# Performance work log

Hardware: AMD Instinct MI355X
Metric: run time of the kernel (lower is better)

The kernel has to match this reference:

```python
import jax, jax.numpy as jnp
import numpy as np

NUM_GRAPHS = 1024
HIDDEN = 256
N_NODES = 500000


def setup_inputs() -> dict:
    key = jax.random.key(0)
    k1, k2, k3, k4 = jax.random.split(key, 4)
    x = jax.random.normal(k1, (N_NODES, HIDDEN), dtype=jnp.float32)
    batch = jnp.sort(jax.random.randint(k2, (N_NODES,), 0, NUM_GRAPHS, dtype=jnp.int64))
    # attention = nn.Linear(hidden_dim, 1): weight [1, hidden], bias [1]
    bound = 1.0 / np.sqrt(HIDDEN)
    att_w = jax.random.uniform(k3, (HIDDEN, 1), dtype=jnp.float32, minval=-bound, maxval=bound)
    att_b = jax.random.uniform(k4, (1,), dtype=jnp.float32, minval=-bound, maxval=bound)
    return {"x": x, "batch": batch, "att_w": att_w, "att_b": att_b}


def reference(x, batch, att_w, att_b):
    seg = batch.astype(jnp.int32)
    # mean pool: segment sum / counts
    sums = jax.ops.segment_sum(x, seg, num_segments=NUM_GRAPHS)  # [G, H]
    counts = jax.ops.segment_sum(jnp.ones((x.shape[0],), x.dtype), seg, num_segments=NUM_GRAPHS)
    mean_pool = sums / jnp.maximum(counts, 1.0)[:, None]
    # max pool
    max_pool = jax.ops.segment_max(x, seg, num_segments=NUM_GRAPHS)
    # attention-weighted add pool: sigmoid(x @ w + b) * x, segment-summed
    weights = jax.nn.sigmoid(x @ att_w + att_b)  # [N, 1]
    att_pool = jax.ops.segment_sum(x * weights, seg, num_segments=NUM_GRAPHS)
    return jnp.concatenate([mean_pool, max_pool, att_pool], axis=-1)
```

## Files before the change

### kernel.cpp

```cpp
#include <hip/hip_runtime.h>
#include <math.h>

constexpr int NUM_GRAPHS = 1024;
constexpr int HIDDEN     = 256;

__global__ void detect_i32_kernel(const int* __restrict__ words, int n,
                                  int* __restrict__ flag) {
    __shared__ int any_nz;
    if (threadIdx.x == 0) any_nz = 0;
    __syncthreads();
    int acc = 0;
    for (int j = 1 + 2 * (int)threadIdx.x; j < n; j += 2 * (int)blockDim.x)
        acc |= words[j];
    if (acc) atomicOr(&any_nz, 1);
    __syncthreads();
    if (threadIdx.x == 0) *flag = any_nz;
}

__global__ void seg_start_kernel(const int* __restrict__ words, int n,
                                 const int* __restrict__ flag,
                                 int* __restrict__ seg) {
    int i = blockIdx.x * blockDim.x + threadIdx.x;
    if (i >= n) return;
    const bool is32 = (*flag != 0);
    int b    = is32 ? words[i] : words[2 * i];
    int prev = (i == 0) ? -1 : (is32 ? words[i - 1] : words[2 * (i - 1)]);
    for (int g = prev + 1; g <= b; ++g) seg[g] = i;
    if (i == n - 1)
        for (int g = b + 1; g <= NUM_GRAPHS; ++g) seg[g] = n;
}

__global__ __launch_bounds__(256) void pool_kernel(
    const float* __restrict__ x, const float* __restrict__ att_w,
    const float* __restrict__ att_b, const int* __restrict__ seg,
    float* __restrict__ out) {
    const int g    = blockIdx.x;
    const int lane = threadIdx.x & 63;
    const int w    = threadIdx.x >> 6;

    const int s0 = seg[g];
    const int e0 = seg[g + 1];

    const float4* __restrict__ x4 = (const float4*)x;
    const float4 wv = ((const float4*)att_w)[lane];
    const float  bias = att_b[0];

    float sx = 0.f, sy = 0.f, sz = 0.f, sw = 0.f;
    float mx = -INFINITY, my = -INFINITY, mz = -INFINITY, mw = -INFINITY;
    float ax = 0.f, ay = 0.f, az = 0.f, aw = 0.f;

    int i = s0 + w;
    if (i < e0) {
        float4 v = x4[(size_t)i * 64 + lane];
        for (;;) {
            const int inext = i + 4;
            float4 vn;
            const bool has_next = (inext < e0);
            if (has_next) vn = x4[(size_t)inext * 64 + lane];

            float p = v.x * wv.x + v.y * wv.y + v.z * wv.z + v.w * wv.w;
#pragma unroll
            for (int off = 32; off >= 1; off >>= 1)
                p += __shfl_xor(p, off, 64);
            const float sig = 1.0f / (1.0f + __expf(-(p + bias)));

            sx += v.x; sy += v.y; sz += v.z; sw += v.w;
            mx = fmaxf(mx, v.x); my = fmaxf(my, v.y);
            mz = fmaxf(mz, v.z); mw = fmaxf(mw, v.w);
            ax += v.x * sig; ay += v.y * sig; az += v.z * sig; aw += v.w * sig;

            if (!has_next) break;
            v = vn;
            i = inext;
        }
    }

    __shared__ float4 lsum[4][64];
    __shared__ float4 lmax[4][64];
    __shared__ float4 latt[4][64];
    lsum[w][lane] = make_float4(sx, sy, sz, sw);
    lmax[w][lane] = make_float4(mx, my, mz, mw);
    latt[w][lane] = make_float4(ax, ay, az, aw);
    __syncthreads();

    if (w == 0) {
        float4 S = lsum[0][lane], M = lmax[0][lane], A = latt[0][lane];
#pragma unroll
        for (int ww = 1; ww < 4; ++ww) {
            float4 s2 = lsum[ww][lane], m2 = lmax[ww][lane], a2 = latt[ww][lane];
            S.x += s2.x; S.y += s2.y; S.z += s2.z; S.w += s2.w;
            M.x = fmaxf(M.x, m2.x); M.y = fmaxf(M.y, m2.y);
            M.z = fmaxf(M.z, m2.z); M.w = fmaxf(M.w, m2.w);
            A.x += a2.x; A.y += a2.y; A.z += a2.z; A.w += a2.w;
        }
        const int cnt = e0 - s0;
        const float inv = 1.0f / (float)(cnt > 0 ? cnt : 1);
        float4* __restrict__ o = (float4*)(out + (size_t)g * 768);
        o[lane]       = make_float4(S.x * inv, S.y * inv, S.z * inv, S.w * inv);
        o[64 + lane]  = M;
        o[128 + lane] = A;
    }
}

extern "C" void kernel_launch(void* const* d_in, const int* in_sizes, int n_in,
                              void* d_out, int out_size, void* d_ws, size_t ws_size,
                              hipStream_t stream) {
    const float* x           = (const float*)d_in[0];
    const int*   batch_words = (const int*)d_in[1];
    const float* att_w       = (const float*)d_in[2];
    const float* att_b       = (const float*)d_in[3];
    float*       out         = (float*)d_out;
    const int n = in_sizes[1];

    int* flag = (int*)d_ws;
    int* seg  = ((int*)d_ws) + 8;

    detect_i32_kernel<<<1, 1024, 0, stream>>>(batch_words, n, flag);
    seg_start_kernel<<<(n + 255) / 256, 256, 0, stream>>>(batch_words, n, flag, seg);
    pool_kernel<<<NUM_GRAPHS, 256, 0, stream>>>(x, att_w, att_b, seg, out);
}
```

Measured before the change: 737.5 us.

## Parallelize dtype detection across blocks and batch four rows per wave in pooling

The int32/int64 detection kernel now runs on 256 blocks with a wave-level any-vote and a global atomicOr, replacing the single 1024-thread block that scanned the whole batch array serially. The flag is cleared with a memset before launch. The pooling loop now loads four rows per wave at once and double-buffers the next four. It also interleaves the four shuffle reductions so more memory loads and shuffles are in flight per wave. The cost is higher register pressure and an extra memset launch.

Measured after the change: 676.8 us. -8.2%, faster.

```diff
diff --git a/kernel.cpp b/kernel.cpp
--- a/kernel.cpp
+++ b/kernel.cpp
@@ -2,19 +2,17 @@
 #include <math.h>
 
 constexpr int NUM_GRAPHS = 1024;
-constexpr int HIDDEN     = 256;
 
 __global__ void detect_i32_kernel(const int* __restrict__ words, int n,
                                   int* __restrict__ flag) {
-    __shared__ int any_nz;
-    if (threadIdx.x == 0) any_nz = 0;
-    __syncthreads();
+    const int stride = gridDim.x * blockDim.x;
     int acc = 0;
-    for (int j = 1 + 2 * (int)threadIdx.x; j < n; j += 2 * (int)blockDim.x)
+    for (int j = 1 + 2 * (int)(blockIdx.x * blockDim.x + threadIdx.x); j < n;
+         j += 2 * stride)
         acc |= words[j];
-    if (acc) atomicOr(&any_nz, 1);
-    __syncthreads();
-    if (threadIdx.x == 0) *flag = any_nz;
+    if (__any(acc != 0)) {
+        if ((threadIdx.x & 63) == 0) atomicOr(flag, 1);
+    }
 }
 
 __global__ void seg_start_kernel(const int* __restrict__ words, int n,
@@ -42,37 +40,66 @@
     const int e0 = seg[g + 1];
 
     const float4* __restrict__ x4 = (const float4*)x;
-    const float4 wv = ((const float4*)att_w)[lane];
+    const float4 wv   = ((const float4*)att_w)[lane];
     const float  bias = att_b[0];
 
     float sx = 0.f, sy = 0.f, sz = 0.f, sw = 0.f;
     float mx = -INFINITY, my = -INFINITY, mz = -INFINITY, mw = -INFINITY;
     float ax = 0.f, ay = 0.f, az = 0.f, aw = 0.f;
 
+    auto proc4 = [&](const float4* v) {
+        float p[4];
+#pragma unroll
+        for (int r = 0; r < 4; ++r)
+            p[r] = v[r].x * wv.x + v[r].y * wv.y + v[r].z * wv.z + v[r].w * wv.w;
+#pragma unroll
+        for (int off = 32; off >= 1; off >>= 1) {
+#pragma unroll
+            for (int r = 0; r < 4; ++r)
+                p[r] += __shfl_xor(p[r], off, 64);
+        }
+#pragma unroll
+        for (int r = 0; r < 4; ++r) {
+            const float sig = 1.0f / (1.0f + __expf(-(p[r] + bias)));
+            sx += v[r].x; sy += v[r].y; sz += v[r].z; sw += v[r].w;
+            mx = fmaxf(mx, v[r].x); my = fmaxf(my, v[r].y);
+            mz = fmaxf(mz, v[r].z); mw = fmaxf(mw, v[r].w);
+            ax += v[r].x * sig; ay += v[r].y * sig;
+            az += v[r].z * sig; aw += v[r].w * sig;
+        }
+    };
+
     int i = s0 + w;
-    if (i < e0) {
-        float4 v = x4[(size_t)i * 64 + lane];
-        for (;;) {
-            const int inext = i + 4;
-            float4 vn;
-            const bool has_next = (inext < e0);
-            if (has_next) vn = x4[(size_t)inext * 64 + lane];
-
-            float p = v.x * wv.x + v.y * wv.y + v.z * wv.z + v.w * wv.w;
+    if (i + 12 < e0) {
+        float4 v[4];
 #pragma unroll
-            for (int off = 32; off >= 1; off >>= 1)
-                p += __shfl_xor(p, off, 64);
-            const float sig = 1.0f / (1.0f + __expf(-(p + bias)));
-
-            sx += v.x; sy += v.y; sz += v.z; sw += v.w;
-            mx = fmaxf(mx, v.x); my = fmaxf(my, v.y);
-            mz = fmaxf(mz, v.z); mw = fmaxf(mw, v.w);
-            ax += v.x * sig; ay += v.y * sig; az += v.z * sig; aw += v.w * sig;
-
-            if (!has_next) break;
-            v = vn;
-            i = inext;
+        for (int r = 0; r < 4; ++r)
+            v[r] = x4[(size_t)(i + 4 * r) * 64 + lane];
+        int nb = i + 16;
+        while (nb + 12 < e0) {
+            float4 vn[4];
+#pragma unroll
+            for (int r = 0; r < 4; ++r)
+                vn[r] = x4[(size_t)(nb + 4 * r) * 64 + lane];
+            proc4(v);
+#pragma unroll
+            for (int r = 0; r < 4; ++r) v[r] = vn[r];
+            nb += 16;
         }
+        proc4(v);
+        i = nb;
+    }
+    for (; i < e0; i += 4) {
+        const float4 v = x4[(size_t)i * 64 + lane];
+        float p = v.x * wv.x + v.y * wv.y + v.z * wv.z + v.w * wv.w;
+#pragma unroll
+        for (int off = 32; off >= 1; off >>= 1)
+            p += __shfl_xor(p, off, 64);
+        const float sig = 1.0f / (1.0f + __expf(-(p + bias)));
+        sx += v.x; sy += v.y; sz += v.z; sw += v.w;
+        mx = fmaxf(mx, v.x); my = fmaxf(my, v.y);
+        mz = fmaxf(mz, v.z); mw = fmaxf(mw, v.w);
+        ax += v.x * sig; ay += v.y * sig; az += v.z * sig; aw += v.w * sig;
     }
 
     __shared__ float4 lsum[4][64];
@@ -115,7 +142,8 @@
     int* flag = (int*)d_ws;
     int* seg  = ((int*)d_ws) + 8;
 
-    detect_i32_kernel<<<1, 1024, 0, stream>>>(batch_words, n, flag);
+    hipMemsetAsync(flag, 0, sizeof(int), stream);
+    detect_i32_kernel<<<256, 256, 0, stream>>>(batch_words, n, flag);
     seg_start_kernel<<<(n + 255) / 256, 256, 0, stream>>>(batch_words, n, flag, seg);
     pool_kernel<<<NUM_GRAPHS, 256, 0, stream>>>(x, att_w, att_b, seg, out);
 }
```
